# Optimization experiments

Measured on AMD Instinct MI355X. Metric: run time of the kernel, lower is better.

Reference implementation:

```python
import jax, jax.numpy as jnp
import numpy as np

B, K, G = 4, 128, 128          # batch, TOP_K_DETECTION (= num proposals), MAX_GT
IMG_H, IMG_W = 480, 640        # original image size used for mask painting
RES_H, RES_W = 24, 32          # resize_with_pad inner size: ratio = max(480/32,640/32)=20
PAD_T = 4                      # (32 - 24)//2 vertical padding
BBOX_STD = jnp.array([0.1, 0.1, 0.2, 0.2], jnp.float32)
# window [128,0,896,1024] normalized per utils.norm_boxes on a 1024x1024 image
_WIN = (jnp.array([128.0, 0.0, 896.0, 1024.0]) - jnp.array([0.0, 0.0, 1.0, 1.0])) / 1023.0
_WSHIFT = jnp.array([_WIN[0], _WIN[1], _WIN[0], _WIN[1]])
_WSCALE = jnp.array([_WIN[2] - _WIN[0], _WIN[3] - _WIN[1], _WIN[2] - _WIN[0], _WIN[3] - _WIN[1]])
_DENORM_SCALE = jnp.array([IMG_H - 1.0, IMG_W - 1.0, IMG_H - 1.0, IMG_W - 1.0])
_DENORM_SHIFT = jnp.array([0.0, 0.0, 1.0, 1.0])


def setup_inputs():
    key = jax.random.key(0)
    kb, kh, kj, kf, kr = jax.random.split(key, 5)
    yx = jax.random.uniform(kb, (B, G, 2), minval=0.05, maxval=0.6)
    hw = jax.random.uniform(kh, (B, G, 2), minval=0.05, maxval=0.35)
    gt_boxes = jnp.concatenate([yx, yx + hw], axis=-1)  # (y1,x1,y2,x2), all non-zero
    p = jnp.clip(gt_boxes + 0.03 * jax.random.normal(kj, (B, G, 4)), 1e-3, 0.999)
    y1 = jnp.minimum(p[..., 0], p[..., 2]); y2 = jnp.maximum(p[..., 0], p[..., 2]) + 1e-3
    x1 = jnp.minimum(p[..., 1], p[..., 3]); x2 = jnp.maximum(p[..., 1], p[..., 3]) + 1e-3
    proposals = jnp.stack([y1, x1, y2, x2], axis=-1)
    obj_feat = jax.random.normal(kf, (B, G, 1, 1, 1024), jnp.float32)
    gt_ranks = jax.random.randint(kr, (B, G), 1, 6, jnp.int32)
    return {"proposals": proposals, "obj_feat": obj_feat, "gt_boxes": gt_boxes, "gt_ranks": gt_ranks}


def _iou(p, g):
    # p: [N,4], g: [M,4] -> [N,M]
    y1 = jnp.maximum(p[:, None, 0], g[None, :, 0])
    x1 = jnp.maximum(p[:, None, 1], g[None, :, 1])
    y2 = jnp.minimum(p[:, None, 2], g[None, :, 2])
    x2 = jnp.minimum(p[:, None, 3], g[None, :, 3])
    inter = jnp.maximum(x2 - x1, 0.0) * jnp.maximum(y2 - y1, 0.0)
    ap = (p[:, 2] - p[:, 0]) * (p[:, 3] - p[:, 1])
    ag = (g[:, 2] - g[:, 0]) * (g[:, 3] - g[:, 1])
    return inter / (ap[:, None] + ag[None, :] - inter)


def _box_refinement(box, gt):
    h = box[:, 2] - box[:, 0]; w = box[:, 3] - box[:, 1]
    cy = box[:, 0] + 0.5 * h;  cx = box[:, 1] + 0.5 * w
    gh = gt[:, 2] - gt[:, 0];  gw = gt[:, 3] - gt[:, 1]
    gcy = gt[:, 0] + 0.5 * gh; gcx = gt[:, 1] + 0.5 * gw
    return jnp.stack([(gcy - cy) / h, (gcx - cx) / w, jnp.log(gh / h), jnp.log(gw / w)], axis=1)


def _spatial_feat(boxes):
    # boxes: [K,4] normalized; returns [K,32,32,1]
    b = (boxes - _WSHIFT) / _WSCALE
    b = jnp.round(b * _DENORM_SCALE + _DENORM_SHIFT).astype(jnp.int32)
    area = (b[:, 2] - b[:, 0]) * (b[:, 3] - b[:, 1])
    b = jnp.where((area > 0)[:, None], b, 0)
    rows = jnp.arange(IMG_H)[None, :, None]
    cols = jnp.arange(IMG_W)[None, None, :]
    y1 = b[:, 0][:, None, None]; x1 = b[:, 1][:, None, None]
    y2 = b[:, 2][:, None, None]; x2 = b[:, 3][:, None, None]
    m = ((y1 < rows) & (x1 < cols) & (rows < y2) & (cols < x2)).astype(jnp.float32)  # [K,480,640]
    r = jax.vmap(lambda im: jax.image.resize(im, (RES_H, RES_W), 'bilinear', antialias=False))(m)
    return jnp.pad(r, ((0, 0), (PAD_T, PAD_T), (0, 0)))[..., None]


def _per_image(props, feat, gtb, gtr):
    feat = feat.reshape(K, -1)                 # squeeze [K,1,1,1024] -> [K,1024]
    iou = _iou(props, gtb)                     # [K,G]
    pos = iou.max(axis=1) >= 0.5
    # stable sort: positives first, original order preserved (== tf.where ordering + concat)
    order = jnp.argsort(jnp.where(pos, 0, 1).astype(jnp.int32), stable=True)
    pos_s = pos[order]
    rois = props[order]
    obj = feat[order][:, None, None, :]
    assign = jnp.argmax(iou, axis=1)
    agt = gtb[assign]
    deltas = jnp.where(pos_s[:, None], (_box_refinement(props, agt) / BBOX_STD)[order], 0.0)
    roi_gt = jnp.where(pos_s[:, None], agt[order], 0.0)
    ranks = jnp.where(pos_s, gtr[assign][order], 0)
    return rois, obj, deltas, ranks, _spatial_feat(roi_gt)


def reference(proposals, obj_feat, gt_boxes, gt_ranks):
    return jax.vmap(_per_image)(proposals, obj_feat, gt_boxes, gt_ranks)
```

## Files before the change

kernel.cpp:

```cpp
#include <hip/hip_runtime.h>

static constexpr int Bn = 4;
static constexpr int Kn = 128;
static constexpr int Gn = 128;

static constexpr int OFF_ROIS   = 0;
static constexpr int OFF_OBJ    = Bn * Kn * 4;
static constexpr int OFF_DELTAS = OFF_OBJ + Bn * Kn * 1024;
static constexpr int OFF_RANKS  = OFF_DELTAS + Bn * Kn * 4;
static constexpr int OFF_SPAT   = OFF_RANKS + Bn * Kn;

static constexpr float W0  = 128.0f / 1023.0f;
static constexpr float W2  = 895.0f / 1023.0f;
static constexpr float WSY = W2 - W0;

__device__ __forceinline__ int cvt_coord(float v, float shift, float scl,
                                         float dscale, float dshift) {
    float t = __fdiv_rn(__fsub_rn(v, shift), scl);
    float u = __fadd_rn(__fmul_rn(t, dscale), dshift);
    return (int)rintf(u);
}

__global__ __launch_bounds__(256)
void k_fused(const float* __restrict__ props, const float* __restrict__ feat,
             const float* __restrict__ gtb, const int* __restrict__ gtr,
             float* __restrict__ out)
{
    const int blk  = blockIdx.x;
    const int b    = blk >> 6;
    const int d0   = (blk & 63) << 1;
    const int t    = threadIdx.x;

    __shared__ float4 sg[Gn];
    __shared__ float  sag[Gn];
    __shared__ float4 spp[Kn];
    __shared__ float  sbest[256];
    __shared__ int    sbj[256];
    __shared__ int    scnt[2];
    __shared__ int    s_src[2];
    __shared__ int4   sbox[2];

    if (t < 128) {
        float4 g = reinterpret_cast<const float4*>(gtb)[b * Gn + t];
        sg[t]  = g;
        sag[t] = __fmul_rn(__fsub_rn(g.z, g.x), __fsub_rn(g.w, g.y));
        spp[t] = reinterpret_cast<const float4*>(props)[b * Kn + t];
    }
    __syncthreads();

    const int i     = t & 127;
    const int jbase = (t >> 7) << 6;
    float4 p  = spp[i];
    float  ap = __fmul_rn(__fsub_rn(p.z, p.x), __fsub_rn(p.w, p.y));
    float best = -1.0f;
    int   bj   = jbase;
    #pragma unroll 4
    for (int jj = 0; jj < 64; ++jj) {
        const int j = jbase + jj;
        float4 q  = sg[j];
        float yy1 = fmaxf(p.x, q.x), xx1 = fmaxf(p.y, q.y);
        float yy2 = fminf(p.z, q.z), xx2 = fminf(p.w, q.w);
        float ih  = fmaxf(__fsub_rn(yy2, yy1), 0.0f);
        float iw  = fmaxf(__fsub_rn(xx2, xx1), 0.0f);
        float inter = __fmul_rn(iw, ih);
        float uni   = __fsub_rn(__fadd_rn(ap, sag[j]), inter);
        float iou   = __fdiv_rn(inter, uni);
        if (iou > best) { best = iou; bj = j; }
    }
    sbest[t] = best;
    sbj[t]   = bj;
    __syncthreads();

    bool pos = false;
    int  bjf = 0;
    if (t < 128) {
        float b0 = sbest[t], b1 = sbest[t + 128];
        bjf = (b0 >= b1) ? sbj[t] : sbj[t + 128];
        pos = (fmaxf(b0, b1) >= 0.5f);
    }

    unsigned long long m = __ballot(pos);
    const int lane = t & 63, wave = t >> 6;
    const int prefix = __popcll(m & ((1ull << lane) - 1ull));
    if (lane == 0 && wave < 2) scnt[wave] = __popcll(m);
    __syncthreads();

    if (t < 128) {
        const int total     = scnt[0] + scnt[1];
        const int posBefore = prefix + (wave ? scnt[0] : 0);
        const int dst_i     = pos ? posBefore : (total + (t - posBefore));
        const int slot      = dst_i - d0;
        if (slot == 0 || slot == 1) {
            s_src[slot] = t;

            float4 agt = sg[bjf];
            float h  = p.z - p.x, w  = p.w - p.y;
            float cy = p.x + 0.5f * h, cx = p.y + 0.5f * w;
            float gh = agt.z - agt.x, gw = agt.w - agt.y;
            float gcy = agt.x + 0.5f * gh, gcx = agt.y + 0.5f * gw;
            float d0f = ((gcy - cy) / h) / 0.1f;
            float d1f = ((gcx - cx) / w) / 0.1f;
            float d2f = logf(gh / h) / 0.2f;
            float d3f = logf(gw / w) / 0.2f;
            float4 deltas = pos ? make_float4(d0f, d1f, d2f, d3f)
                                : make_float4(0.f, 0.f, 0.f, 0.f);
            float4 rg = pos ? agt : make_float4(0.f, 0.f, 0.f, 0.f);

            int ib0 = cvt_coord(rg.x, W0, WSY, 479.0f, 0.0f);
            int ib1 = cvt_coord(rg.y, 0.0f, 1.0f, 639.0f, 0.0f);
            int ib2 = cvt_coord(rg.z, W0, WSY, 479.0f, 1.0f);
            int ib3 = cvt_coord(rg.w, 0.0f, 1.0f, 639.0f, 1.0f);
            int area = (ib2 - ib0) * (ib3 - ib1);
            if (!(area > 0)) { ib0 = 0; ib1 = 0; ib2 = 0; ib3 = 0; }
            sbox[slot] = make_int4(ib0, ib1, ib2, ib3);

            const int o = b * Kn + dst_i;
            reinterpret_cast<float4*>(out + OFF_ROIS)[o]   = p;
            reinterpret_cast<float4*>(out + OFF_DELTAS)[o] = deltas;
            out[OFF_RANKS + o] = (float)(pos ? gtr[b * Gn + bjf] : 0);
        }
    }
    __syncthreads();

    #pragma unroll
    for (int slot = 0; slot < 2; ++slot) {
        const int  o   = b * Kn + d0 + slot;
        const int  src = s_src[slot];
        const int4 bb  = sbox[slot];

        const float4* srow = reinterpret_cast<const float4*>(feat) + (b * Gn + src) * 256;
        reinterpret_cast<float4*>(out + OFF_OBJ)[o * 256 + t] = srow[t];

        const int p0      = t * 4;
        const int row     = p0 >> 5;
        const int colBase = p0 & 31;
        float4 sp = make_float4(0.f, 0.f, 0.f, 0.f);
        if (row >= 4 && row < 28) {
            const int r   = row - 4;
            const int ys0 = 20 * r + 9, ys1 = ys0 + 1;
            const int fy  = (int)((bb.x < ys0) & (ys0 < bb.z)) +
                            (int)((bb.x < ys1) & (ys1 < bb.z));
            if (fy) {
                float v[4];
                #pragma unroll
                for (int q = 0; q < 4; ++q) {
                    const int c   = colBase + q;
                    const int xs0 = 20 * c + 9, xs1 = xs0 + 1;
                    const int fx  = (int)((bb.y < xs0) & (xs0 < bb.w)) +
                                    (int)((bb.y < xs1) & (xs1 < bb.w));
                    v[q] = 0.25f * (float)(fy * fx);
                }
                sp = make_float4(v[0], v[1], v[2], v[3]);
            }
        }
        reinterpret_cast<float4*>(out + OFF_SPAT)[o * 256 + t] = sp;
    }
}

extern "C" void kernel_launch(void* const* d_in, const int* in_sizes, int n_in,
                              void* d_out, int out_size, void* d_ws, size_t ws_size,
                              hipStream_t stream) {
    (void)in_sizes; (void)n_in; (void)out_size; (void)d_ws; (void)ws_size;
    const float* props = (const float*)d_in[0];
    const float* feat  = (const float*)d_in[1];
    const float* gtb   = (const float*)d_in[2];
    const int*   gtr   = (const int*)d_in[3];
    float* out = (float*)d_out;

    k_fused<<<(Bn * Kn) / 2, 256, 0, stream>>>(props, feat, gtb, gtr, out);
}
```

Baseline: 13.35 us.

## Replace full IoU argmax with division-free positive test and per-slot argmax

Each thread now checks whether any IoU reaches the 0.5 threshold using a double-precision multiply comparison instead of a rounded division and argmax over all 128 GT boxes. GT boxes are read as wave-uniform scalar loads from global memory. The exact argmax is then recomputed only for the two source proposals that land in this block's output slots, using a wave shuffle reduction. This removes most per-element divisions and the shared-memory merge, at the cost of double-precision compares and a threshold constant chosen to match float rounding, which may differ from the original at boundary cases.

Result: slower. 14.86 us (+11.3%).

```diff
diff --git a/kernel.cpp b/kernel.cpp
--- a/kernel.cpp
+++ b/kernel.cpp
@@ -13,6 +13,8 @@
 static constexpr float W0  = 128.0f / 1023.0f;
 static constexpr float W2  = 895.0f / 1023.0f;
 static constexpr float WSY = W2 - W0;
+
+static constexpr double CTH = 0.5 - 1.4901161193847656e-08;
 
 __device__ __forceinline__ int cvt_coord(float v, float shift, float scl,
                                          float dscale, float dshift) {
@@ -30,13 +32,12 @@
     const int b    = blk >> 6;
     const int d0   = (blk & 63) << 1;
     const int t    = threadIdx.x;
+    const int lane = t & 63, wave = t >> 6;
 
     __shared__ float4 sg[Gn];
     __shared__ float  sag[Gn];
     __shared__ float4 spp[Kn];
-    __shared__ float  sbest[256];
-    __shared__ int    sbj[256];
-    __shared__ int    scnt[2];
+    __shared__ unsigned long long sbal[4];
     __shared__ int    s_src[2];
     __shared__ int4   sbox[2];
 
@@ -52,50 +53,74 @@
     const int jbase = (t >> 7) << 6;
     float4 p  = spp[i];
     float  ap = __fmul_rn(__fsub_rn(p.z, p.x), __fsub_rn(p.w, p.y));
-    float best = -1.0f;
-    int   bj   = jbase;
+    const float* gq = gtb + (size_t)(b * Gn + __builtin_amdgcn_readfirstlane(jbase)) * 4;
+    bool found = false;
     #pragma unroll 4
     for (int jj = 0; jj < 64; ++jj) {
-        const int j = jbase + jj;
-        float4 q  = sg[j];
-        float yy1 = fmaxf(p.x, q.x), xx1 = fmaxf(p.y, q.y);
-        float yy2 = fminf(p.z, q.z), xx2 = fminf(p.w, q.w);
+        float qx = gq[4 * jj + 0], qy = gq[4 * jj + 1];
+        float qz = gq[4 * jj + 2], qw = gq[4 * jj + 3];
+        float yy1 = fmaxf(p.x, qx), xx1 = fmaxf(p.y, qy);
+        float yy2 = fminf(p.z, qz), xx2 = fminf(p.w, qw);
         float ih  = fmaxf(__fsub_rn(yy2, yy1), 0.0f);
         float iw  = fmaxf(__fsub_rn(xx2, xx1), 0.0f);
         float inter = __fmul_rn(iw, ih);
-        float uni   = __fsub_rn(__fadd_rn(ap, sag[j]), inter);
-        float iou   = __fdiv_rn(inter, uni);
-        if (iou > best) { best = iou; bj = j; }
+        float uni   = __fsub_rn(__fadd_rn(ap, sag[jbase + jj]), inter);
+        found |= ((double)inter >= CTH * (double)uni);
     }
-    sbest[t] = best;
-    sbj[t]   = bj;
+    unsigned long long bal = __ballot(found);
+    if (lane == 0) sbal[wave] = bal;
     __syncthreads();
 
-    bool pos = false;
-    int  bjf = 0;
-    if (t < 128) {
-        float b0 = sbest[t], b1 = sbest[t + 128];
-        bjf = (b0 >= b1) ? sbj[t] : sbj[t + 128];
-        pos = (fmaxf(b0, b1) >= 0.5f);
-    }
+    if (wave < 2) {
+        const unsigned long long m01 = sbal[0] | sbal[2];
+        const unsigned long long m23 = sbal[1] | sbal[3];
+        const int nPos   = __popcll(m01) + __popcll(m23);
+        const int target = d0 + wave;
+        const unsigned long long lm = (lane == 63) ? ~0ull >> 1 : ((1ull << lane) - 1ull);
+        const unsigned long long lmask = (1ull << lane) - 1ull;
+        (void)lm;
+        const int pos1 = (int)((m01 >> lane) & 1ull);
+        const int pb1  = __popcll(m01 & lmask);
+        const int dst1 = pos1 ? pb1 : nPos + (lane - pb1);
+        const int pos2 = (int)((m23 >> lane) & 1ull);
+        const int pb2  = __popcll(m01) + __popcll(m23 & lmask);
+        const int dst2 = pos2 ? pb2 : nPos + (lane + 64 - pb2);
 
-    unsigned long long m = __ballot(pos);
-    const int lane = t & 63, wave = t >> 6;
-    const int prefix = __popcll(m & ((1ull << lane) - 1ull));
-    if (lane == 0 && wave < 2) scnt[wave] = __popcll(m);
-    __syncthreads();
+        const unsigned long long b1 = __ballot(dst1 == target);
+        const unsigned long long b2 = __ballot(dst2 == target);
+        int src, spos;
+        if (b1) { int l = __ffsll((long long)b1) - 1; src = l;      spos = (int)((m01 >> l) & 1ull); }
+        else    { int l = __ffsll((long long)b2) - 1; src = 64 + l; spos = (int)((m23 >> l) & 1ull); }
 
-    if (t < 128) {
-        const int total     = scnt[0] + scnt[1];
-        const int posBefore = prefix + (wave ? scnt[0] : 0);
-        const int dst_i     = pos ? posBefore : (total + (t - posBefore));
-        const int slot      = dst_i - d0;
-        if (slot == 0 || slot == 1) {
-            s_src[slot] = t;
+        float4 ps  = spp[src];
+        float  aps = __fmul_rn(__fsub_rn(ps.z, ps.x), __fsub_rn(ps.w, ps.y));
+        float v[2]; int jj2[2] = { lane, lane + 64 };
+        #pragma unroll
+        for (int h = 0; h < 2; ++h) {
+            const int j = jj2[h];
+            float4 q  = sg[j];
+            float yy1 = fmaxf(ps.x, q.x), xx1 = fmaxf(ps.y, q.y);
+            float yy2 = fminf(ps.z, q.z), xx2 = fminf(ps.w, q.w);
+            float ih  = fmaxf(__fsub_rn(yy2, yy1), 0.0f);
+            float iw  = fmaxf(__fsub_rn(xx2, xx1), 0.0f);
+            float inter = __fmul_rn(iw, ih);
+            float uni   = __fsub_rn(__fadd_rn(aps, sag[j]), inter);
+            v[h] = __fdiv_rn(inter, uni);
+        }
+        float bv = v[0]; int bj = lane;
+        if (v[1] > bv) { bv = v[1]; bj = lane + 64; }
+        #pragma unroll
+        for (int off = 1; off < 64; off <<= 1) {
+            float ov = __shfl_xor(bv, off);
+            int   oj = __shfl_xor(bj, off);
+            if (ov > bv || (ov == bv && oj < bj)) { bv = ov; bj = oj; }
+        }
 
-            float4 agt = sg[bjf];
-            float h  = p.z - p.x, w  = p.w - p.y;
-            float cy = p.x + 0.5f * h, cx = p.y + 0.5f * w;
+        if (lane == 0) {
+            const bool pos = (spos != 0);
+            float4 agt = sg[bj];
+            float h  = ps.z - ps.x, w  = ps.w - ps.y;
+            float cy = ps.x + 0.5f * h, cx = ps.y + 0.5f * w;
             float gh = agt.z - agt.x, gw = agt.w - agt.y;
             float gcy = agt.x + 0.5f * gh, gcx = agt.y + 0.5f * gw;
             float d0f = ((gcy - cy) / h) / 0.1f;
@@ -112,12 +137,13 @@
             int ib3 = cvt_coord(rg.w, 0.0f, 1.0f, 639.0f, 1.0f);
             int area = (ib2 - ib0) * (ib3 - ib1);
             if (!(area > 0)) { ib0 = 0; ib1 = 0; ib2 = 0; ib3 = 0; }
-            sbox[slot] = make_int4(ib0, ib1, ib2, ib3);
 
-            const int o = b * Kn + dst_i;
-            reinterpret_cast<float4*>(out + OFF_ROIS)[o]   = p;
+            const int o = b * Kn + target;
+            reinterpret_cast<float4*>(out + OFF_ROIS)[o]   = ps;
             reinterpret_cast<float4*>(out + OFF_DELTAS)[o] = deltas;
-            out[OFF_RANKS + o] = (float)(pos ? gtr[b * Gn + bjf] : 0);
+            out[OFF_RANKS + o] = (float)(pos ? gtr[b * Gn + bj] : 0);
+            s_src[wave] = src;
+            sbox[wave]  = make_int4(ib0, ib1, ib2, ib3);
         }
     }
     __syncthreads();
@@ -141,16 +167,16 @@
             const int fy  = (int)((bb.x < ys0) & (ys0 < bb.z)) +
                             (int)((bb.x < ys1) & (ys1 < bb.z));
             if (fy) {
-                float v[4];
+                float vv[4];
                 #pragma unroll
                 for (int q = 0; q < 4; ++q) {
                     const int c   = colBase + q;
                     const int xs0 = 20 * c + 9, xs1 = xs0 + 1;
                     const int fx  = (int)((bb.y < xs0) & (xs0 < bb.w)) +
                                     (int)((bb.y < xs1) & (xs1 < bb.w));
-                    v[q] = 0.25f * (float)(fy * fx);
+                    vv[q] = 0.25f * (float)(fy * fx);
                 }
-                sp = make_float4(v[0], v[1], v[2], v[3]);
+                sp = make_float4(vv[0], vv[1], vv[2], vv[3]);
             }
         }
         reinterpret_cast<float4*>(out + OFF_SPAT)[o * 256 + t] = sp;
```
